# Kernel optimization log

Hardware: AMD Instinct MI355X
Metric: run time of the kernel (lower is better)

Reference implementation:

```python
import jax, jax.numpy as jnp
import numpy as np

BN_EPS = 1e-5
K2 = 9  # 3x3 kernel


def _conv3x3(x, w, b):
    # x: [B,C,H,W], w: [O,C,3,3] -> [B,O,H,W], stride 1, pad 1
    out = jax.lax.conv_general_dilated(
        x, w, window_strides=(1, 1), padding=((1, 1), (1, 1)),
        dimension_numbers=("NCHW", "OIHW", "NCHW"))
    return out + b[None, :, None, None]


def setup_inputs() -> dict:
    key = jax.random.key(0)
    ks = jax.random.split(key, 8)
    B, C, H, W = 8, 256, 64, 64
    O = 256
    x = jax.random.normal(ks[0], (B, C, H, W), dtype=jnp.float32)
    # offset/mask conv: small init so sampled offsets stay near the base grid
    w_off = jax.random.normal(ks[1], (3 * K2, C, 3, 3), dtype=jnp.float32) * 0.01
    b_off = jnp.zeros((3 * K2,), dtype=jnp.float32)
    weight = jax.random.normal(ks[2], (O, C, 3, 3), dtype=jnp.float32) * 0.02
    bias = jnp.zeros((O,), dtype=jnp.float32)
    gamma = jnp.ones((O,), dtype=jnp.float32)
    beta = jnp.zeros((O,), dtype=jnp.float32)
    run_mean = jax.random.normal(ks[3], (O,), dtype=jnp.float32) * 0.1
    run_var = jax.random.uniform(ks[4], (O,), dtype=jnp.float32) + 0.5
    return {"x": x, "w_off": w_off, "b_off": b_off, "weight": weight,
            "bias": bias, "gamma": gamma, "beta": beta,
            "run_mean": run_mean, "run_var": run_var}


def _deform_sample(img, py, px):
    # img: [C,H,W]; py, px: [K2,H,W] sampling coordinates.
    # Bilinear sample with zero padding outside (DCNv2 semantics:
    # out-of-bounds corners contribute zero).
    C, H, W = img.shape
    y0 = jnp.floor(py)
    x0 = jnp.floor(px)
    wy1 = py - y0  # frac weights for the 'high' corner
    wx1 = px - x0

    def gather(yi, xi):
        valid = (yi >= 0) & (yi < H) & (xi >= 0) & (xi < W)
        yc = jnp.clip(yi, 0, H - 1).astype(jnp.int32)
        xc = jnp.clip(xi, 0, W - 1).astype(jnp.int32)
        return img[:, yc, xc] * valid.astype(img.dtype)[None]  # [C,K2,H,W]

    v00 = gather(y0, x0)
    v01 = gather(y0, x0 + 1)
    v10 = gather(y0 + 1, x0)
    v11 = gather(y0 + 1, x0 + 1)
    return (v00 * ((1 - wy1) * (1 - wx1))[None]
            + v01 * ((1 - wy1) * wx1)[None]
            + v10 * (wy1 * (1 - wx1))[None]
            + v11 * (wy1 * wx1)[None])  # [C,K2,H,W]


def reference(x, w_off, b_off, weight, bias, gamma, beta, run_mean, run_var):
    B, C, H, W = x.shape
    O = weight.shape[0]
    # 1) offset / mask branch (standard 3x3 conv)
    om = _conv3x3(x, w_off, b_off)  # [B, 27, H, W]
    off_y = om[:, :K2]
    off_x = om[:, K2:2 * K2]
    mask = jax.nn.sigmoid(om[:, 2 * K2:])  # modulation, [B,9,H,W]
    # 2) base sampling grid for 3x3, stride 1, pad 1, dilation 1
    ky = jnp.repeat(jnp.arange(3), 3).astype(x.dtype)  # [9]
    kx = jnp.tile(jnp.arange(3), 3).astype(x.dtype)    # [9]
    hs = jnp.arange(H, dtype=x.dtype)
    ws = jnp.arange(W, dtype=x.dtype)
    base_y = hs[None, :, None] - 1.0 + ky[:, None, None]  # [9,H,1]
    base_x = ws[None, None, :] - 1.0 + kx[:, None, None]  # [9,1,W]
    py = base_y[None] + off_y  # [B,9,H,W]
    px = base_x[None] + off_x
    # 3) modulated deformable im2col (bilinear gather) per batch
    cols = jax.vmap(_deform_sample)(x, py, px)  # [B,C,9,H,W]
    cols = cols * mask[:, None]                 # apply modulation mask
    # 4) GEMM over (C, K2) + bias
    w3 = weight.reshape(O, C, K2)
    out = jnp.einsum("ock,bckhw->bohw", w3, cols) + bias[None, :, None, None]
    # 5) BatchNorm (eval mode, running stats) + ReLU
    inv = gamma / jnp.sqrt(run_var + BN_EPS)
    out = out * inv[None, :, None, None] + (beta - run_mean * inv)[None, :, None, None]
    return jax.nn.relu(out)
```

## Files before the change

### kernel.cpp

```cpp
#include <hip/hip_runtime.h>
#include <math.h>

#define H 64
#define W 64
#define C 256
#define O 256
#define CK 2304
#define NB 8
#define HWSZ 4096

typedef __attribute__((ext_vector_type(8))) short short8;
typedef __attribute__((ext_vector_type(4))) float floatx4;
typedef __attribute__((ext_vector_type(4))) unsigned uintx4;

#define FSWZ(n) ((((n) & 3) << 1) | (((n) >> 2) & 1))

__device__ __forceinline__ unsigned short f2bf(float f) {
  unsigned u = __builtin_bit_cast(unsigned, f);
  unsigned r = (u + 0x7fffu + ((u >> 16) & 1u)) >> 16;
  return (unsigned short)r;
}
__device__ __forceinline__ float lo2f(unsigned u) {
  return __builtin_bit_cast(float, u << 16);
}
__device__ __forceinline__ float hi2f(unsigned u) {
  return __builtin_bit_cast(float, u & 0xffff0000u);
}
__device__ __forceinline__ unsigned pk2bf(float v0, float v1) {
  unsigned a = __builtin_bit_cast(unsigned, v0);
  unsigned b = __builtin_bit_cast(unsigned, v1);
  return ((a + 0x8000u) >> 16) | ((b + 0x8000u) & 0xffff0000u);
}

__global__ __launch_bounds__(256) void transpose_x(
    const float* __restrict__ x, unsigned short* __restrict__ xt) {
  __shared__ unsigned tile[64 * 65];
  int b = blockIdx.x, y = blockIdx.y, cg = blockIdx.z;
  int tid = threadIdx.x;
  const float* xb = x + ((size_t)b * C + cg * 128) * HWSZ + y * W;
#pragma unroll 4
  for (int it = 0; it < 16; ++it) {
    int e = tid + 256 * it;
    int xx = e & 63;
    int cp = e >> 6;
    float f0 = xb[(size_t)(2 * cp) * HWSZ + xx];
    float f1 = xb[(size_t)(2 * cp + 1) * HWSZ + xx];
    tile[cp * 65 + xx] = (unsigned)f2bf(f0) | ((unsigned)f2bf(f1) << 16);
  }
  __syncthreads();
  unsigned short* xo = xt + ((size_t)(b * 64 + y) << 14) + cg * 128;
#pragma unroll
  for (int it = 0; it < 4; ++it) {
    int e = tid + 256 * it;
    int cq = e & 15;
    int xx = e >> 4;
    unsigned u0 = tile[(cq * 4 + 0) * 65 + xx];
    unsigned u1 = tile[(cq * 4 + 1) * 65 + xx];
    unsigned u2 = tile[(cq * 4 + 2) * 65 + xx];
    unsigned u3 = tile[(cq * 4 + 3) * 65 + xx];
    uint4 v = {u0, u1, u2, u3};
    *reinterpret_cast<uint4*>(xo + (xx << 8) + (cq << 3)) = v;
  }
}

__global__ __launch_bounds__(256) void prep_weight(
    const float* __restrict__ weight, unsigned short* __restrict__ wb) {
  int d0 = (blockIdx.x * 256 + threadIdx.x) * 2;
  unsigned short v[2];
#pragma unroll
  for (int e = 0; e < 2; ++e) {
    int d = d0 + e;
    int j = d & 7;
    int lane = (d >> 3) & 63;
    int mt = (d >> 9) & 15;
    int ks = d >> 13;
    int o = mt * 16 + (lane & 15);
    int kn = ks * 32 + (lane >> 4) * 8 + j;
    int tap = kn >> 8;
    int c = kn & 255;
    v[e] = f2bf(weight[o * CK + c * 9 + tap]);
  }
  *reinterpret_cast<unsigned*>(wb + d0) =
      (unsigned)v[0] | ((unsigned)v[1] << 16);
}

__global__ __launch_bounds__(256) void prep_woff(
    const float* __restrict__ w_off, unsigned short* __restrict__ wob) {
  int d0 = (blockIdx.x * 256 + threadIdx.x) * 2;
  unsigned short v[2];
#pragma unroll
  for (int e = 0; e < 2; ++e) {
    int d = d0 + e;
    int j = d & 7;
    int lane = (d >> 3) & 63;
    int mt = (d >> 9) & 1;
    int ks = d >> 10;
    int o = mt * 16 + (lane & 15);
    int kn = ks * 32 + (lane >> 4) * 8 + j;
    int tap = kn >> 8;
    int c = kn & 255;
    v[e] = (o < 27) ? f2bf(w_off[o * CK + c * 9 + tap]) : (unsigned short)0;
  }
  *reinterpret_cast<unsigned*>(wob + d0) =
      (unsigned)v[0] | ((unsigned)v[1] << 16);
}

__global__ __launch_bounds__(256) void prep_bn(
    const float* __restrict__ bias, const float* __restrict__ gamma,
    const float* __restrict__ beta, const float* __restrict__ run_mean,
    const float* __restrict__ run_var, float* __restrict__ invsh) {
  int o = threadIdx.x;
  float inv = gamma[o] * rsqrtf(run_var[o] + 1e-5f);
  invsh[o] = inv;
  invsh[O + o] = beta[o] + (bias[o] - run_mean[o]) * inv;
}

__global__ __launch_bounds__(512, 4) void deform_mfma_kernel(
    const unsigned short* __restrict__ xt, const unsigned short* __restrict__ wob,
    const float* __restrict__ b_off, const unsigned short* __restrict__ wb,
    const float* __restrict__ invsh, float* __restrict__ out) {
  __shared__ short cols[64 * 256];
  __shared__ float sm_om[27 * 64];
  __shared__ int sbase[576];
  __shared__ float s00[576], s01[576], s10[576], s11[576];

  int tid = threadIdx.x;
  int lane = tid & 63;
  int wvid = tid >> 6;
  int q = lane >> 4;
  int lm = lane & 15;
  int b = blockIdx.x;
  int h = blockIdx.y;
  const unsigned short* xtb = xt + ((size_t)b << 20);

  {
    int mt = wvid & 1;
    int nt = wvid >> 1;
    floatx4 acc0 = (floatx4){0.f, 0.f, 0.f, 0.f};
    int px = nt * 16 + lm;
    for (int tap = 0; tap < 9; ++tap) {
      int yy = h - 1 + tap / 3;
      int xx = px - 1 + tap % 3;
      bool v = (yy >= 0) && (yy < H) && (xx >= 0) && (xx < W);
      const unsigned short* bp =
          xtb + ((((yy & 63) << 6) + (xx & 63)) << 8) + q * 8;
#pragma unroll
      for (int s = 0; s < 8; ++s) {
        int ks = tap * 8 + s;
        short8 bfrag;
        if (v)
          bfrag = *reinterpret_cast<const short8*>(bp + s * 32);
        else
          bfrag = (short8){0, 0, 0, 0, 0, 0, 0, 0};
        short8 afrag = *reinterpret_cast<const short8*>(
            wob + (((ks * 2 + mt) * 64 + lane) << 3));
        acc0 = __builtin_amdgcn_mfma_f32_16x16x32_bf16(afrag, bfrag, acc0, 0, 0, 0);
      }
    }
#pragma unroll
    for (int r = 0; r < 4; ++r) {
      int o = mt * 16 + q * 4 + r;
      if (o < 27) sm_om[o * 64 + px] = acc0[r] + b_off[o];
    }
  }
  __syncthreads();

  for (int e = tid; e < 576; e += 512) {
    int n = e & 63;
    int k = e >> 6;
    float oy = sm_om[k * 64 + n];
    float ox = sm_om[(9 + k) * 64 + n];
    float mv = sm_om[(18 + k) * 64 + n];
    float m = 1.0f / (1.0f + __expf(-mv));
    float py = (float)(h - 1 + k / 3) + oy;
    float px = (float)(n - 1 + k % 3) + ox;
    float yf = floorf(py), xf = floorf(px);
    int y0 = (int)yf, x0 = (int)xf;
    float fy = py - yf, fx = px - xf;
    float r0, r1; int yl;
    if (y0 >= 0 && y0 <= H - 2)      { yl = y0;    r0 = 1.f - fy; r1 = fy;       }
    else if (y0 == -1)               { yl = 0;     r0 = fy;       r1 = 0.f;      }
    else if (y0 == H - 1)            { yl = H - 2; r0 = 0.f;      r1 = 1.f - fy; }
    else                             { yl = 0;     r0 = 0.f;      r1 = 0.f;      }
    float c0, c1; int xl;
    if (x0 >= 0 && x0 <= W - 2)      { xl = x0;    c0 = 1.f - fx; c1 = fx;       }
    else if (x0 == -1)               { xl = 0;     c0 = fx;       c1 = 0.f;      }
    else if (x0 == W - 1)            { xl = W - 2; c0 = 0.f;      c1 = 1.f - fx; }
    else                             { xl = 0;     c0 = 0.f;      c1 = 0.f;      }
    r0 *= m; r1 *= m;
    sbase[e] = ((yl << 6) + xl) << 8;
    s00[e] = r0 * c0; s01[e] = r0 * c1;
    s10[e] = r1 * c0; s11[e] = r1 * c1;
  }
  __syncthreads();

  floatx4 acc[4][2];
  int mg = wvid >> 1;
  int nh = wvid & 1;
#pragma unroll
  for (int a = 0; a < 4; ++a)
#pragma unroll
    for (int u = 0; u < 2; ++u) acc[a][u] = (floatx4){0.f, 0.f, 0.f, 0.f};

  int sn = tid >> 3;
  int scb = tid & 7;

  for (int tap = 0; tap < 9; ++tap) {
    if (tap) __syncthreads();
    {
      int ei = tap * 64 + sn;
      int base = sbase[ei];
      float w00 = s00[ei], w01 = s01[ei], w10 = s10[ei], w11 = s11[ei];
      const unsigned short* p = xtb + base;
#pragma unroll
      for (int i = 0; i < 4; ++i) {
        int cbw = (i << 3) | scb;
        int co = cbw << 3;
        uintx4 u00 = *reinterpret_cast<const uintx4*>(p + co);
        uintx4 u01 = *reinterpret_cast<const uintx4*>(p + 256 + co);
        uintx4 u10 = *reinterpret_cast<const uintx4*>(p + 16384 + co);
        uintx4 u11 = *reinterpret_cast<const uintx4*>(p + 16640 + co);
        uintx4 res;
#pragma unroll
        for (int jd = 0; jd < 4; ++jd) {
          float v0 = fmaf(w00, lo2f(u00[jd]),
                     fmaf(w01, lo2f(u01[jd]),
                     fmaf(w10, lo2f(u10[jd]), w11 * lo2f(u11[jd]))));
          float v1 = fmaf(w00, hi2f(u00[jd]),
                     fmaf(w01, hi2f(u01[jd]),
                     fmaf(w10, hi2f(u10[jd]), w11 * hi2f(u11[jd]))));
          res[jd] = pk2bf(v0, v1);
        }
        int pos = (cbw ^ FSWZ(sn)) & 31;
        *reinterpret_cast<uintx4*>(&cols[(sn << 8) + (pos << 3)]) = res;
      }
    }
    __syncthreads();

#pragma unroll
    for (int s = 0; s < 8; ++s) {
      int ks = tap * 8 + s;
      short8 afrag[4];
#pragma unroll
      for (int a = 0; a < 4; ++a)
        afrag[a] = *reinterpret_cast<const short8*>(
            wb + (((ks * 16 + mg * 4 + a) * 64 + lane) << 3));
      short8 bfrag[2];
#pragma unroll
      for (int u = 0; u < 2; ++u) {
        int nn = (nh * 2 + u) * 16 + lm;
        int pos = ((s * 4 + q) ^ FSWZ(nn)) & 31;
        bfrag[u] = *reinterpret_cast<const short8*>(&cols[(nn << 8) + (pos << 3)]);
      }
#pragma unroll
      for (int a = 0; a < 4; ++a)
#pragma unroll
        for (int u = 0; u < 2; ++u)
          acc[a][u] = __builtin_amdgcn_mfma_f32_16x16x32_bf16(
              afrag[a], bfrag[u], acc[a][u], 0, 0, 0);
    }
  }

#pragma unroll
  for (int a = 0; a < 4; ++a) {
#pragma unroll
    for (int u = 0; u < 2; ++u) {
      int nn = (nh * 2 + u) * 16 + lm;
#pragma unroll
      for (int r = 0; r < 4; ++r) {
        int o = (mg * 4 + a) * 16 + q * 4 + r;
        float v = fmaf(acc[a][u][r], invsh[o], invsh[O + o]);
        out[((size_t)(b * O + o)) * HWSZ + h * W + nn] = fmaxf(v, 0.0f);
      }
    }
  }
}

extern "C" void kernel_launch(void* const* d_in, const int* in_sizes, int n_in,
                              void* d_out, int out_size, void* d_ws, size_t ws_size,
                              hipStream_t stream) {
  const float* x        = (const float*)d_in[0];
  const float* w_off    = (const float*)d_in[1];
  const float* b_off    = (const float*)d_in[2];
  const float* weight   = (const float*)d_in[3];
  const float* bias     = (const float*)d_in[4];
  const float* gamma    = (const float*)d_in[5];
  const float* beta     = (const float*)d_in[6];
  const float* run_mean = (const float*)d_in[7];
  const float* run_var  = (const float*)d_in[8];
  float* out = (float*)d_out;

  char* ws = (char*)d_ws;
  unsigned short* xt = (unsigned short*)ws;
  unsigned short* wbf = (unsigned short*)(ws + 16777216);
  unsigned short* wob = (unsigned short*)(ws + 17956864);
  float* invsh = (float*)(ws + 18104320);

  {
    dim3 grid(NB, H, 2);
    transpose_x<<<grid, 256, 0, stream>>>(x, xt);
  }
  prep_weight<<<O * CK / 512, 256, 0, stream>>>(weight, wbf);
  prep_woff<<<32 * CK / 512, 256, 0, stream>>>(w_off, wob);
  prep_bn<<<1, 256, 0, stream>>>(bias, gamma, beta, run_mean, run_var, invsh);

  {
    dim3 grid(NB, H);
    deform_mfma_kernel<<<grid, 512, 0, stream>>>(xt, wob, b_off, wbf, invsh, out);
  }
}
```

Measured before the change: 208.7 us.

## Merge prep kernels into one launch and retile offset and main GEMM waves

```diff
diff --git a/kernel.cpp b/kernel.cpp
--- a/kernel.cpp
+++ b/kernel.cpp
@@ -32,87 +32,93 @@
   return ((a + 0x8000u) >> 16) | ((b + 0x8000u) & 0xffff0000u);
 }
 
-__global__ __launch_bounds__(256) void transpose_x(
-    const float* __restrict__ x, unsigned short* __restrict__ xt) {
+__global__ __launch_bounds__(256) void prep_all(
+    const float* __restrict__ x, const float* __restrict__ weight,
+    const float* __restrict__ w_off, const float* __restrict__ bias,
+    const float* __restrict__ gamma, const float* __restrict__ beta,
+    const float* __restrict__ run_mean, const float* __restrict__ run_var,
+    unsigned short* __restrict__ xt, unsigned short* __restrict__ wb,
+    unsigned short* __restrict__ wob, float* __restrict__ invsh) {
   __shared__ unsigned tile[64 * 65];
-  int b = blockIdx.x, y = blockIdx.y, cg = blockIdx.z;
+  int bid = blockIdx.x;
   int tid = threadIdx.x;
-  const float* xb = x + ((size_t)b * C + cg * 128) * HWSZ + y * W;
-#pragma unroll 4
-  for (int it = 0; it < 16; ++it) {
-    int e = tid + 256 * it;
-    int xx = e & 63;
-    int cp = e >> 6;
-    float f0 = xb[(size_t)(2 * cp) * HWSZ + xx];
-    float f1 = xb[(size_t)(2 * cp + 1) * HWSZ + xx];
-    tile[cp * 65 + xx] = (unsigned)f2bf(f0) | ((unsigned)f2bf(f1) << 16);
-  }
-  __syncthreads();
-  unsigned short* xo = xt + ((size_t)(b * 64 + y) << 14) + cg * 128;
-#pragma unroll
-  for (int it = 0; it < 4; ++it) {
-    int e = tid + 256 * it;
-    int cq = e & 15;
-    int xx = e >> 4;
-    unsigned u0 = tile[(cq * 4 + 0) * 65 + xx];
-    unsigned u1 = tile[(cq * 4 + 1) * 65 + xx];
-    unsigned u2 = tile[(cq * 4 + 2) * 65 + xx];
-    unsigned u3 = tile[(cq * 4 + 3) * 65 + xx];
-    uint4 v = {u0, u1, u2, u3};
-    *reinterpret_cast<uint4*>(xo + (xx << 8) + (cq << 3)) = v;
-  }
-}
-
-__global__ __launch_bounds__(256) void prep_weight(
-    const float* __restrict__ weight, unsigned short* __restrict__ wb) {
-  int d0 = (blockIdx.x * 256 + threadIdx.x) * 2;
-  unsigned short v[2];
-#pragma unroll
-  for (int e = 0; e < 2; ++e) {
-    int d = d0 + e;
-    int j = d & 7;
-    int lane = (d >> 3) & 63;
-    int mt = (d >> 9) & 15;
-    int ks = d >> 13;
+
+  if (bid < 1024) {
+    int b = bid & 7;
+    int t = bid >> 3;
+    int y = t >> 1;
+    int cg = t & 1;
+    const float* xb = x + ((size_t)b * C + cg * 128) * HWSZ + y * W;
+#pragma unroll
+    for (int it = 0; it < 4; ++it) {
+      int e = tid + 256 * it;
+      int xx4 = e & 15;
+      int cp = e >> 4;
+      floatx4 f0 = *reinterpret_cast<const floatx4*>(
+          xb + (size_t)(2 * cp) * HWSZ + xx4 * 4);
+      floatx4 f1 = *reinterpret_cast<const floatx4*>(
+          xb + (size_t)(2 * cp + 1) * HWSZ + xx4 * 4);
+#pragma unroll
+      for (int k = 0; k < 4; ++k)
+        tile[cp * 65 + xx4 * 4 + k] = pk2bf(f0[k], f1[k]);
+    }
+    __syncthreads();
+    unsigned short* xo = xt + ((size_t)(b * 64 + y) << 14) + cg * 128;
+#pragma unroll
+    for (int it = 0; it < 4; ++it) {
+      int e = tid + 256 * it;
+      int cq = e & 15;
+      int xx = e >> 4;
+      unsigned u0 = tile[(cq * 4 + 0) * 65 + xx];
+      unsigned u1 = tile[(cq * 4 + 1) * 65 + xx];
+      unsigned u2 = tile[(cq * 4 + 2) * 65 + xx];
+      unsigned u3 = tile[(cq * 4 + 3) * 65 + xx];
+      uint4 v = {u0, u1, u2, u3};
+      *reinterpret_cast<uint4*>(xo + (xx << 8) + (cq << 3)) = v;
+    }
+  } else if (bid < 1312) {
+    int d0 = ((bid - 1024) * 256 + tid) * 8;
+    int lane = (d0 >> 3) & 63;
+    int mt = (d0 >> 9) & 15;
+    int ks = d0 >> 13;
     int o = mt * 16 + (lane & 15);
-    int kn = ks * 32 + (lane >> 4) * 8 + j;
-    int tap = kn >> 8;
-    int c = kn & 255;
-    v[e] = f2bf(weight[o * CK + c * 9 + tap]);
-  }
-  *reinterpret_cast<unsigned*>(wb + d0) =
-      (unsigned)v[0] | ((unsigned)v[1] << 16);
-}
-
-__global__ __launch_bounds__(256) void prep_woff(
-    const float* __restrict__ w_off, unsigned short* __restrict__ wob) {
-  int d0 = (blockIdx.x * 256 + threadIdx.x) * 2;
-  unsigned short v[2];
-#pragma unroll
-  for (int e = 0; e < 2; ++e) {
-    int d = d0 + e;
-    int j = d & 7;
-    int lane = (d >> 3) & 63;
-    int mt = (d >> 9) & 1;
-    int ks = d >> 10;
+    int kn0 = ks * 32 + (lane >> 4) * 8;
+    int tap = kn0 >> 8;
+    int c0 = kn0 & 255;
+    const float* wsrc = weight + o * CK + c0 * 9 + tap;
+    unsigned pk[4];
+#pragma unroll
+    for (int p = 0; p < 4; ++p)
+      pk[p] = pk2bf(wsrc[(2 * p) * 9], wsrc[(2 * p + 1) * 9]);
+    uint4 v = {pk[0], pk[1], pk[2], pk[3]};
+    *reinterpret_cast<uint4*>(wb + d0) = v;
+  } else if (bid < 1348) {
+    int d0 = ((bid - 1312) * 256 + tid) * 8;
+    int lane = (d0 >> 3) & 63;
+    int mt = (d0 >> 9) & 1;
+    int ks = d0 >> 10;
     int o = mt * 16 + (lane & 15);
-    int kn = ks * 32 + (lane >> 4) * 8 + j;
-    int tap = kn >> 8;
-    int c = kn & 255;
-    v[e] = (o < 27) ? f2bf(w_off[o * CK + c * 9 + tap]) : (unsigned short)0;
-  }
-  *reinterpret_cast<unsigned*>(wob + d0) =
-      (unsigned)v[0] | ((unsigned)v[1] << 16);
-}
-
-__global__ __launch_bounds__(256) void prep_bn(
-    const float* __restrict__ bias, const float* __restrict__ gamma,
-    const float* __restrict__ beta, const float* __restrict__ run_mean,
-    const float* __restrict__ run_var, float* __restrict__ invsh) {
-  int o = threadIdx.x;
-  float inv = gamma[o] * rsqrtf(run_var[o] + 1e-5f);
-  invsh[o] = inv;
-  invsh[O + o] = beta[o] + (bias[o] - run_mean[o]) * inv;
+    int kn0 = ks * 32 + (lane >> 4) * 8;
+    int tap = kn0 >> 8;
+    int c0 = kn0 & 255;
+    uint4 v;
+    if (o < 27) {
+      const float* wsrc = w_off + o * CK + c0 * 9 + tap;
+      unsigned pk[4];
+#pragma unroll
+      for (int p = 0; p < 4; ++p)
+        pk[p] = pk2bf(wsrc[(2 * p) * 9], wsrc[(2 * p + 1) * 9]);
+      v = (uint4){pk[0], pk[1], pk[2], pk[3]};
+    } else {
+      v = (uint4){0, 0, 0, 0};
+    }
+    *reinterpret_cast<uint4*>(wob + d0) = v;
+  } else {
+    int o = tid;
+    float inv = gamma[o] * rsqrtf(run_var[o] + 1e-5f);
+    invsh[o] = inv;
+    invsh[O + o] = beta[o] + (bias[o] - run_mean[o]) * inv;
+  }
 }
 
 __global__ __launch_bounds__(512, 4) void deform_mfma_kernel(
@@ -133,35 +139,49 @@
   int h = blockIdx.y;
   const unsigned short* xtb = xt + ((size_t)b << 20);
 
-  {
+  if (wvid < 4) {
     int mt = wvid & 1;
-    int nt = wvid >> 1;
-    floatx4 acc0 = (floatx4){0.f, 0.f, 0.f, 0.f};
-    int px = nt * 16 + lm;
+    int nh = wvid >> 1;
+    floatx4 a0[2];
+    a0[0] = (floatx4){0.f, 0.f, 0.f, 0.f};
+    a0[1] = (floatx4){0.f, 0.f, 0.f, 0.f};
+    int pxu[2];
+    pxu[0] = (nh * 2 + 0) * 16 + lm;
+    pxu[1] = (nh * 2 + 1) * 16 + lm;
     for (int tap = 0; tap < 9; ++tap) {
       int yy = h - 1 + tap / 3;
-      int xx = px - 1 + tap % 3;
-      bool v = (yy >= 0) && (yy < H) && (xx >= 0) && (xx < W);
-      const unsigned short* bp =
-          xtb + ((((yy & 63) << 6) + (xx & 63)) << 8) + q * 8;
+      bool vy = (yy >= 0) && (yy < H);
+      const unsigned short* bp[2];
+      bool vv[2];
+#pragma unroll
+      for (int u = 0; u < 2; ++u) {
+        int xx = pxu[u] - 1 + tap % 3;
+        vv[u] = vy && (xx >= 0) && (xx < W);
+        bp[u] = xtb + ((((yy & 63) << 6) + (xx & 63)) << 8) + q * 8;
+      }
 #pragma unroll
       for (int s = 0; s < 8; ++s) {
         int ks = tap * 8 + s;
-        short8 bfrag;
-        if (v)
-          bfrag = *reinterpret_cast<const short8*>(bp + s * 32);
-        else
-          bfrag = (short8){0, 0, 0, 0, 0, 0, 0, 0};
         short8 afrag = *reinterpret_cast<const short8*>(
             wob + (((ks * 2 + mt) * 64 + lane) << 3));
-        acc0 = __builtin_amdgcn_mfma_f32_16x16x32_bf16(afrag, bfrag, acc0, 0, 0, 0);
-      }
-    }
-#pragma unroll
-    for (int r = 0; r < 4; ++r) {
-      int o = mt * 16 + q * 4 + r;
-      if (o < 27) sm_om[o * 64 + px] = acc0[r] + b_off[o];
-    }
+#pragma unroll
+        for (int u = 0; u < 2; ++u) {
+          short8 bfrag;
+          if (vv[u])
+            bfrag = *reinterpret_cast<const short8*>(bp[u] + s * 32);
+          else
+            bfrag = (short8){0, 0, 0, 0, 0, 0, 0, 0};
+          a0[u] = __builtin_amdgcn_mfma_f32_16x16x32_bf16(afrag, bfrag, a0[u], 0, 0, 0);
+        }
+      }
+    }
+#pragma unroll
+    for (int u = 0; u < 2; ++u)
+#pragma unroll
+      for (int r = 0; r < 4; ++r) {
+        int o = mt * 16 + q * 4 + r;
+        if (o < 27) sm_om[o * 64 + pxu[u]] = a0[u][r] + b_off[o];
+      }
   }
   __syncthreads();
 
@@ -194,13 +214,11 @@
   }
   __syncthreads();
 
-  floatx4 acc[4][2];
-  int mg = wvid >> 1;
-  int nh = wvid & 1;
-#pragma unroll
-  for (int a = 0; a < 4; ++a)
-#pragma unroll
-    for (int u = 0; u < 2; ++u) acc[a][u] = (floatx4){0.f, 0.f, 0.f, 0.f};
+  floatx4 acc[2][4];
+#pragma unroll
+  for (int a = 0; a < 2; ++a)
+#pragma unroll
+    for (int u = 0; u < 4; ++u) acc[a][u] = (floatx4){0.f, 0.f, 0.f, 0.f};
 
   int sn = tid >> 3;
   int scb = tid & 7;
@@ -240,35 +258,35 @@
 #pragma unroll
     for (int s = 0; s < 8; ++s) {
       int ks = tap * 8 + s;
-      short8 afrag[4];
-#pragma unroll
-      for (int a = 0; a < 4; ++a)
+      short8 afrag[2];
+#pragma unroll
+      for (int a = 0; a < 2; ++a)
         afrag[a] = *reinterpret_cast<const short8*>(
-            wb + (((ks * 16 + mg * 4 + a) * 64 + lane) << 3));
-      short8 bfrag[2];
-#pragma unroll
-      for (int u = 0; u < 2; ++u) {
-        int nn = (nh * 2 + u) * 16 + lm;
+            wb + (((ks * 16 + wvid * 2 + a) * 64 + lane) << 3));
+      short8 bfrag[4];
+#pragma unroll
+      for (int u = 0; u < 4; ++u) {
+        int nn = u * 16 + lm;
         int pos = ((s * 4 + q) ^ FSWZ(nn)) & 31;
         bfrag[u] = *reinterpret_cast<const short8*>(&cols[(nn << 8) + (pos << 3)]);
       }
 #pragma unroll
-      for (int a = 0; a < 4; ++a)
-#pragma unroll
-        for (int u = 0; u < 2; ++u)
+      for (int a = 0; a < 2; ++a)
+#pragma unroll
+        for (int u = 0; u < 4; ++u)
           acc[a][u] = __builtin_amdgcn_mfma_f32_16x16x32_bf16(
               afrag[a], bfrag[u], acc[a][u], 0, 0, 0);
     }
   }
 
 #pragma unroll
-  for (int a = 0; a < 4; ++a) {
-#pragma unroll
-    for (int u = 0; u < 2; ++u) {
-      int nn = (nh * 2 + u) * 16 + lm;
+  for (int a = 0; a < 2; ++a) {
+#pragma unroll
+    for (int u = 0; u < 4; ++u) {
+      int nn = u * 16 + lm;
 #pragma unroll
       for (int r = 0; r < 4; ++r) {
-        int o = (mg * 4 + a) * 16 + q * 4 + r;
+        int o = (wvid * 2 + a) * 16 + q * 4 + r;
         float v = fmaf(acc[a][u][r], invsh[o], invsh[O + o]);
         out[((size_t)(b * O + o)) * HWSZ + h * W + nn] = fmaxf(v, 0.0f);
       }
@@ -296,14 +314,8 @@
   unsigned short* wob = (unsigned short*)(ws + 17956864);
   float* invsh = (float*)(ws + 18104320);
 
-  {
-    dim3 grid(NB, H, 2);
-    transpose_x<<<grid, 256, 0, stream>>>(x, xt);
-  }
-  prep_weight<<<O * CK / 512, 256, 0, stream>>>(weight, wbf);
-  prep_woff<<<32 * CK / 512, 256, 0, stream>>>(w_off, wob);
-  prep_bn<<<1, 256, 0, stream>>>(bias, gamma, beta, run_mean, run_var, invsh);
-
+  prep_all<<<1349, 256, 0, stream>>>(x, weight, w_off, bias, gamma, beta,
+                                     run_mean, run_var, xt, wbf, wob, invsh);
   {
     dim3 grid(NB, H);
     deform_mfma_kernel<<<grid, 512, 0, stream>>>(xt, wob, b_off, wbf, invsh, out);
```

Result: faster. 192.5 us (-7.8%).
